# Kernel optimization log

Measured on AMD Instinct MI355X. Metric: run time of the kernel, lower is better.

Reference implementation:

```python
import jax, jax.numpy as jnp
import numpy as np

REG1 = 0.05
REG2 = 0.05
EPS = 1e-12  # clamp before sqrt for numerical safety (matches cdist >= 0)


def setup_inputs() -> dict:
    key = jax.random.key(0)
    k1, k2 = jax.random.split(key)
    N, P, D = 65536, 512, 256
    z = jax.random.normal(k1, (N, D), dtype=jnp.float32)
    prototype_vectors = jax.random.normal(k2, (P, D), dtype=jnp.float32)
    return {"z": z, "prototype_vectors": prototype_vectors}


def _pairwise_dist(z, protos):
    # Euclidean cdist via ||z||^2 + ||p||^2 - 2 z.p^T, computed ONCE.
    z2 = jnp.sum(z * z, axis=-1)          # [N]
    p2 = jnp.sum(protos * protos, axis=-1)  # [P]
    sq = z2[:, None] + p2[None, :] - 2.0 * jnp.einsum('nd,pd->np', z, protos)
    return jnp.sqrt(jnp.maximum(sq, EPS))  # [N, P]


def reference(z, prototype_vectors):
    dist = _pairwise_dist(z, prototype_vectors)  # [N, P]
    # p_dist.min(1).mean(): for each sample, nearest prototype
    p_term = jnp.mean(jnp.min(dist, axis=1))
    # f_dist = cdist(protos, z) = dist.T; its min over axis 1 == dist.min(axis=0)
    f_term = jnp.mean(jnp.min(dist, axis=0))
    return REG1 * p_term + REG2 * f_term
```

## Files before the change

kernel.cpp:

```cpp
#include <hip/hip_runtime.h>

#define NTOT 65536
#define PTOT 512
#define DTOT 256
#define BM   64
#define BK   32
#define NK   (DTOT / BK)
#define GRID_MAIN (NTOT / BM)
#define EPSQ 1e-12f

typedef _Float16 f16x8 __attribute__((ext_vector_type(8)));
typedef _Float16 f16x4 __attribute__((ext_vector_type(4)));
typedef float    f32x4 __attribute__((ext_vector_type(4)));

#define WS_P2      262144
#define WS_COLPART 264192
#define WS_ROWPART 2361344
#define WS_FMINSQ  2365440

__device__ __forceinline__ void gload_lds16(const void* g, void* l) {
  __builtin_amdgcn_global_load_lds((const __attribute__((address_space(1))) void*)g,
                                   (__attribute__((address_space(3))) void*)l,
                                   16, 0, 0);
}

__device__ __forceinline__ f16x8 cvt8(const float4 a, const float4 b, float& zsq) {
  f16x8 h;
  h[0] = (_Float16)a.x; h[1] = (_Float16)a.y; h[2] = (_Float16)a.z; h[3] = (_Float16)a.w;
  h[4] = (_Float16)b.x; h[5] = (_Float16)b.y; h[6] = (_Float16)b.z; h[7] = (_Float16)b.w;
#pragma unroll
  for (int i = 0; i < 8; ++i) { float f = (float)h[i]; zsq = fmaf(f, f, zsq); }
  return h;
}

__global__ __launch_bounds__(64) void proto_prep_k(const float* __restrict__ protos,
                                                   _Float16* __restrict__ protosH,
                                                   float* __restrict__ p2) {
  const int p = blockIdx.x;
  const int l = threadIdx.x;
  const float4 v = *reinterpret_cast<const float4*>(protos + (size_t)p * DTOT + l * 4);
  f16x4 h;
  h[0] = (_Float16)v.x; h[1] = (_Float16)v.y; h[2] = (_Float16)v.z; h[3] = (_Float16)v.w;
  *reinterpret_cast<f16x4*>(protosH + (size_t)p * DTOT + l * 4) = h;
  float s = 0.f;
#pragma unroll
  for (int i = 0; i < 4; ++i) { float f = (float)h[i]; s = fmaf(f, f, s); }
#pragma unroll
  for (int m = 1; m < 64; m <<= 1) s += __shfl_xor(s, m, 64);
  if (l == 0) p2[p] = s;
}

__global__ __launch_bounds__(256, 2) void pdist_main_k(const float* __restrict__ z,
                                                       const _Float16* __restrict__ protosH,
                                                       const float* __restrict__ p2g,
                                                       float* __restrict__ colpart,
                                                       float* __restrict__ rowpart) {
  __shared__ _Float16 Plds[2][PTOT * BK];
  __shared__ _Float16 Zlds[2][BM * BK];
  __shared__ float zsqs[BM];
  __shared__ float rowmin_s[4][BM];

  const int t    = threadIdx.x;
  const int lane = t & 63;
  const int wid  = t >> 6;
  const int bid  = blockIdx.x;

  const int srow = t >> 2;
  const int sg   = t & 3;
  const float* zsrc = z + (size_t)(bid * BM + srow) * DTOT + sg * 8;
  const _Float16* psrc = protosH + (size_t)(wid * 128 + (lane >> 2)) * DTOT + (lane & 3) * 8;
  char* pldsb0 = reinterpret_cast<char*>(&Plds[0][0]) + wid * 8192;
  char* pldsb1 = reinterpret_cast<char*>(&Plds[1][0]) + wid * 8192;

  float zsq = 0.f;

  f32x4 acc[4][8];
#pragma unroll
  for (int a = 0; a < 4; ++a)
#pragma unroll
    for (int b = 0; b < 8; ++b) acc[a][b] = (f32x4)0.f;

  {
    float4 va = *reinterpret_cast<const float4*>(zsrc);
    float4 vb = *reinterpret_cast<const float4*>(zsrc + 4);
#pragma unroll
    for (int j = 0; j < 8; ++j)
      gload_lds16(psrc + j * 16 * DTOT, pldsb0 + j * 1024);
    f16x8 h = cvt8(va, vb, zsq);
    *reinterpret_cast<f16x8*>(&Zlds[0][srow * BK + sg * 8]) = h;
  }
  __syncthreads();

  const int fr = lane & 15;
  const int fg = lane >> 4;
#pragma unroll
  for (int kb = 0; kb < NK; ++kb) {
    const int cur = kb & 1;
    float4 va, vb;
    if (kb + 1 < NK) {
      va = *reinterpret_cast<const float4*>(zsrc + (kb + 1) * BK);
      vb = *reinterpret_cast<const float4*>(zsrc + (kb + 1) * BK + 4);
#pragma unroll
      for (int j = 0; j < 8; ++j)
        gload_lds16(psrc + j * 16 * DTOT + (kb + 1) * BK,
                    (cur ? pldsb0 : pldsb1) + j * 1024);
    }

    f16x8 afrag[4], bfrag[8];
#pragma unroll
    for (int rf = 0; rf < 4; ++rf)
      afrag[rf] = *reinterpret_cast<const f16x8*>(
          &Zlds[cur][(rf * 16 + fr) * BK + fg * 8]);
#pragma unroll
    for (int cf = 0; cf < 8; ++cf)
      bfrag[cf] = *reinterpret_cast<const f16x8*>(
          &Plds[cur][(wid * 128 + cf * 16 + fr) * BK + fg * 8]);
#pragma unroll
    for (int rf = 0; rf < 4; ++rf)
#pragma unroll
      for (int cf = 0; cf < 8; ++cf)
        acc[rf][cf] = __builtin_amdgcn_mfma_f32_16x16x32_f16(afrag[rf], bfrag[cf],
                                                             acc[rf][cf], 0, 0, 0);

    if (kb + 1 < NK) {
      f16x8 h = cvt8(va, vb, zsq);
      *reinterpret_cast<f16x8*>(&Zlds[cur ^ 1][srow * BK + sg * 8]) = h;
    }
    __syncthreads();
  }

  zsq += __shfl_xor(zsq, 1, 64);
  zsq += __shfl_xor(zsq, 2, 64);
  if (sg == 0) zsqs[srow] = zsq;
  __syncthreads();

  float p2l[8];
#pragma unroll
  for (int cf = 0; cf < 8; ++cf) p2l[cf] = p2g[wid * 128 + cf * 16 + fr];
  float zl[4][4];
#pragma unroll
  for (int rf = 0; rf < 4; ++rf)
#pragma unroll
    for (int r = 0; r < 4; ++r) zl[rf][r] = zsqs[rf * 16 + fg * 4 + r];

  float rowm[4][4], colm[8];
#pragma unroll
  for (int rf = 0; rf < 4; ++rf)
#pragma unroll
    for (int r = 0; r < 4; ++r) rowm[rf][r] = 3.4e38f;
#pragma unroll
  for (int cf = 0; cf < 8; ++cf) colm[cf] = 3.4e38f;

#pragma unroll
  for (int rf = 0; rf < 4; ++rf)
#pragma unroll
    for (int cf = 0; cf < 8; ++cf) {
      f32x4 a = acc[rf][cf];
#pragma unroll
      for (int r = 0; r < 4; ++r) {
        float sq = fmaxf(zl[rf][r] + p2l[cf] - 2.f * a[r], EPSQ);
        rowm[rf][r] = fminf(rowm[rf][r], sq);
        colm[cf]    = fminf(colm[cf], sq);
      }
    }

#pragma unroll
  for (int m = 1; m <= 8; m <<= 1)
#pragma unroll
    for (int rf = 0; rf < 4; ++rf)
#pragma unroll
      for (int r = 0; r < 4; ++r)
        rowm[rf][r] = fminf(rowm[rf][r], __shfl_xor(rowm[rf][r], m, 64));
  if (fr == 0)
#pragma unroll
    for (int rf = 0; rf < 4; ++rf)
#pragma unroll
      for (int r = 0; r < 4; ++r)
        rowmin_s[wid][rf * 16 + fg * 4 + r] = rowm[rf][r];

#pragma unroll
  for (int m = 16; m <= 32; m <<= 1)
#pragma unroll
    for (int cf = 0; cf < 8; ++cf)
      colm[cf] = fminf(colm[cf], __shfl_xor(colm[cf], m, 64));
  if (fg == 0)
#pragma unroll
    for (int cf = 0; cf < 8; ++cf)
      colpart[(size_t)bid * PTOT + wid * 128 + cf * 16 + fr] = colm[cf];
  __syncthreads();

  if (t < BM) {
    float m = fminf(fminf(rowmin_s[0][t], rowmin_s[1][t]),
                    fminf(rowmin_s[2][t], rowmin_s[3][t]));
    float d = sqrtf(m);
#pragma unroll
    for (int mm = 1; mm < 64; mm <<= 1) d += __shfl_xor(d, mm, 64);
    if (t == 0) rowpart[bid] = d;
  }
}

__global__ __launch_bounds__(256) void reduce_cols_k(const float* __restrict__ colpart,
                                                     float* __restrict__ fmin_sq) {
  const int p = blockIdx.x;
  const int t = threadIdx.x;
  float m = 3.4e38f;
#pragma unroll
  for (int j = 0; j < 4; ++j)
    m = fminf(m, colpart[(size_t)(j * 256 + t) * PTOT + p]);
#pragma unroll
  for (int mm = 1; mm < 64; mm <<= 1) m = fminf(m, __shfl_xor(m, mm, 64));
  __shared__ float red[4];
  if ((t & 63) == 0) red[t >> 6] = m;
  __syncthreads();
  if (t == 0)
    fmin_sq[p] = fminf(fminf(red[0], red[1]), fminf(red[2], red[3]));
}

__global__ __launch_bounds__(512) void finalize_k(const float* __restrict__ fmin_sq,
                                                  const float* __restrict__ rowpart,
                                                  float* __restrict__ out) {
  const int t = threadIdx.x, lane = t & 63, wid = t >> 6;
  float fs = sqrtf(fmin_sq[t]);
  float ps = rowpart[t] + rowpart[t + 512];
#pragma unroll
  for (int mm = 1; mm < 64; mm <<= 1) {
    fs += __shfl_xor(fs, mm, 64);
    ps += __shfl_xor(ps, mm, 64);
  }
  __shared__ float red[2][8];
  if (lane == 0) { red[0][wid] = fs; red[1][wid] = ps; }
  __syncthreads();
  if (t == 0) {
    float F = 0.f, P = 0.f;
#pragma unroll
    for (int w = 0; w < 8; ++w) { F += red[0][w]; P += red[1][w]; }
    out[0] = 0.05f * (P / (float)NTOT) + 0.05f * (F / (float)PTOT);
  }
}

extern "C" void kernel_launch(void* const* d_in, const int* in_sizes, int n_in,
                              void* d_out, int out_size, void* d_ws, size_t ws_size,
                              hipStream_t stream) {
  const float* z      = (const float*)d_in[0];
  const float* protos = (const float*)d_in[1];
  float* out = (float*)d_out;

  char* ws = (char*)d_ws;
  _Float16* protosH = (_Float16*)ws;
  float* p2      = (float*)(ws + WS_P2);
  float* colpart = (float*)(ws + WS_COLPART);
  float* rowpart = (float*)(ws + WS_ROWPART);
  float* fmin_sq = (float*)(ws + WS_FMINSQ);

  proto_prep_k<<<PTOT, 64, 0, stream>>>(protos, protosH, p2);
  pdist_main_k<<<GRID_MAIN, 256, 0, stream>>>(z, protosH, p2, colpart, rowpart);
  reduce_cols_k<<<PTOT, 256, 0, stream>>>(colpart, fmin_sq);
  finalize_k<<<1, 512, 0, stream>>>(fmin_sq, rowpart, out);
}
```

Before: 131.7 us.

## Load prototype B-fragments directly to registers and transpose colpart layout

Stops staging the fp16 prototype tile through LDS and has each wave load its MFMA B-fragments straight from global memory (L2-resident) into registers, prefetching the next K-slice. This frees 64KB of LDS per block, which could raise occupancy, and replaces __syncthreads with a manual lgkmcnt wait plus s_barrier. The column-min partials are also stored transposed, so the column-reduction kernel reads contiguously instead of with a stride. The risks are exposed global-load latency for the B operand and more VGPR pressure from the prefetched fragments.

```diff
diff --git a/kernel.cpp b/kernel.cpp
--- a/kernel.cpp
+++ b/kernel.cpp
@@ -17,12 +17,6 @@
 #define WS_COLPART 264192
 #define WS_ROWPART 2361344
 #define WS_FMINSQ  2365440
-
-__device__ __forceinline__ void gload_lds16(const void* g, void* l) {
-  __builtin_amdgcn_global_load_lds((const __attribute__((address_space(1))) void*)g,
-                                   (__attribute__((address_space(3))) void*)l,
-                                   16, 0, 0);
-}
 
 __device__ __forceinline__ f16x8 cvt8(const float4 a, const float4 b, float& zsq) {
   f16x8 h;
@@ -55,7 +49,6 @@
                                                        const float* __restrict__ p2g,
                                                        float* __restrict__ colpart,
                                                        float* __restrict__ rowpart) {
-  __shared__ _Float16 Plds[2][PTOT * BK];
   __shared__ _Float16 Zlds[2][BM * BK];
   __shared__ float zsqs[BM];
   __shared__ float rowmin_s[4][BM];
@@ -65,12 +58,15 @@
   const int wid  = t >> 6;
   const int bid  = blockIdx.x;
 
+  const int fr = lane & 15;
+  const int fg = lane >> 4;
+
   const int srow = t >> 2;
   const int sg   = t & 3;
   const float* zsrc = z + (size_t)(bid * BM + srow) * DTOT + sg * 8;
-  const _Float16* psrc = protosH + (size_t)(wid * 128 + (lane >> 2)) * DTOT + (lane & 3) * 8;
-  char* pldsb0 = reinterpret_cast<char*>(&Plds[0][0]) + wid * 8192;
-  char* pldsb1 = reinterpret_cast<char*>(&Plds[1][0]) + wid * 8192;
+
+  const f16x8* pB = reinterpret_cast<const f16x8*>(protosH) +
+                    ((size_t)(wid * 128 + fr) * (DTOT / 8) + fg);
 
   float zsq = 0.f;
 
@@ -79,54 +75,49 @@
   for (int a = 0; a < 4; ++a)
 #pragma unroll
     for (int b = 0; b < 8; ++b) acc[a][b] = (f32x4)0.f;
+
+  f16x8 bfr[8];
 
   {
     float4 va = *reinterpret_cast<const float4*>(zsrc);
     float4 vb = *reinterpret_cast<const float4*>(zsrc + 4);
 #pragma unroll
-    for (int j = 0; j < 8; ++j)
-      gload_lds16(psrc + j * 16 * DTOT, pldsb0 + j * 1024);
+    for (int cf = 0; cf < 8; ++cf) bfr[cf] = pB[cf * 512];
     f16x8 h = cvt8(va, vb, zsq);
     *reinterpret_cast<f16x8*>(&Zlds[0][srow * BK + sg * 8]) = h;
   }
   __syncthreads();
 
-  const int fr = lane & 15;
-  const int fg = lane >> 4;
 #pragma unroll
   for (int kb = 0; kb < NK; ++kb) {
     const int cur = kb & 1;
+
+    f16x8 afrag[4];
+#pragma unroll
+    for (int rf = 0; rf < 4; ++rf)
+      afrag[rf] = *reinterpret_cast<const f16x8*>(&Zlds[cur][(rf * 16 + fr) * BK + fg * 8]);
+
     float4 va, vb;
     if (kb + 1 < NK) {
       va = *reinterpret_cast<const float4*>(zsrc + (kb + 1) * BK);
       vb = *reinterpret_cast<const float4*>(zsrc + (kb + 1) * BK + 4);
-#pragma unroll
-      for (int j = 0; j < 8; ++j)
-        gload_lds16(psrc + j * 16 * DTOT + (kb + 1) * BK,
-                    (cur ? pldsb0 : pldsb1) + j * 1024);
     }
 
-    f16x8 afrag[4], bfrag[8];
-#pragma unroll
-    for (int rf = 0; rf < 4; ++rf)
-      afrag[rf] = *reinterpret_cast<const f16x8*>(
-          &Zlds[cur][(rf * 16 + fr) * BK + fg * 8]);
-#pragma unroll
-    for (int cf = 0; cf < 8; ++cf)
-      bfrag[cf] = *reinterpret_cast<const f16x8*>(
-          &Plds[cur][(wid * 128 + cf * 16 + fr) * BK + fg * 8]);
 #pragma unroll
     for (int rf = 0; rf < 4; ++rf)
 #pragma unroll
       for (int cf = 0; cf < 8; ++cf)
-        acc[rf][cf] = __builtin_amdgcn_mfma_f32_16x16x32_f16(afrag[rf], bfrag[cf],
+        acc[rf][cf] = __builtin_amdgcn_mfma_f32_16x16x32_f16(afrag[rf], bfr[cf],
                                                              acc[rf][cf], 0, 0, 0);
 
     if (kb + 1 < NK) {
+#pragma unroll
+      for (int cf = 0; cf < 8; ++cf) bfr[cf] = pB[cf * 512 + (kb + 1) * 4];
       f16x8 h = cvt8(va, vb, zsq);
       *reinterpret_cast<f16x8*>(&Zlds[cur ^ 1][srow * BK + sg * 8]) = h;
+      asm volatile("s_waitcnt lgkmcnt(0)" ::: "memory");
+      __builtin_amdgcn_s_barrier();
     }
-    __syncthreads();
   }
 
   zsq += __shfl_xor(zsq, 1, 64);
@@ -186,7 +177,7 @@
   if (fg == 0)
 #pragma unroll
     for (int cf = 0; cf < 8; ++cf)
-      colpart[(size_t)bid * PTOT + wid * 128 + cf * 16 + fr] = colm[cf];
+      colpart[(size_t)(wid * 128 + cf * 16 + fr) * GRID_MAIN + bid] = colm[cf];
   __syncthreads();
 
   if (t < BM) {
@@ -203,10 +194,11 @@
                                                      float* __restrict__ fmin_sq) {
   const int p = blockIdx.x;
   const int t = threadIdx.x;
+  const float* row = colpart + (size_t)p * GRID_MAIN;
   float m = 3.4e38f;
 #pragma unroll
   for (int j = 0; j < 4; ++j)
-    m = fminf(m, colpart[(size_t)(j * 256 + t) * PTOT + p]);
+    m = fminf(m, row[j * 256 + t]);
 #pragma unroll
   for (int mm = 1; mm < 64; mm <<= 1) m = fminf(m, __shfl_xor(m, mm, 64));
   __shared__ float red[4];
```

Result: slower. 145.8 us (+10.7%).
